# Kernel optimization log

Measured on AMD Instinct MI355X. Metric: run time of the kernel, lower is better.

## Reference

```python
import jax, jax.numpy as jnp
import numpy as np

B_, N, F_ = 8, 2048, 64
H_ = F_ // 2          # hidden state size = 32
DIM = H_ + 2          # LocalGC r/u feature size = 34
NEG = -1e16


def setup_inputs() -> dict:
    key = jax.random.key(0)
    ks = jax.random.split(key, 16)
    xav = lambda k, shp: jax.random.normal(k, shp, jnp.float32) * 0.02
    eye = jnp.eye(N, dtype=jnp.float32)
    A = jnp.maximum((jax.random.uniform(ks[0], (N, N)) < 0.05).astype(jnp.float32), eye)
    Badj = jnp.maximum((jax.random.uniform(ks[1], (N, N)) < 0.05).astype(jnp.float32), eye)
    return dict(
        input=jax.random.normal(ks[2], (B_, N, 2), jnp.float32),
        state=jax.random.normal(ks[3], (B_, N, H_), jnp.float32),
        A=A, Badj=Badj,
        w1c=xav(ks[4], (2, F_, N)), w2c=xav(ks[5], (2, N, N)), biasc=jnp.zeros((2, N, 1)),
        convW=xav(ks[6], (F_, 2)), convb=jnp.zeros((2,)),
        linin_W=xav(ks[7], (2, H_)), linin_b=jnp.zeros((H_,)),
        wr=xav(ks[8], (N, N)), br=jnp.zeros((DIM,)),
        linr_W=xav(ks[9], (DIM, H_)), linr_b=jnp.zeros((H_,)),
        wu=xav(ks[10], (N, N)), bu=jnp.zeros((DIM,)),
        linu_W=xav(ks[11], (DIM, H_)), linu_b=jnp.zeros((H_,)),
        wc=xav(ks[12], (N, N)), bc=jnp.zeros((F_,)),
        linc_W=xav(ks[13], (F_, H_)), linc_b=jnp.zeros((H_,)),
    )


def _local_gc(x, adj, w, b):
    # x: [B,N,D]; out[b,m,d] = sum_n x[b,n,d] * (adj*w)[n,m] + b[d]
    return jnp.einsum('bnd,nm->bmd', x, adj * w) + b


def _core(g, inp, A, Badj, w1c, w2c, biasc, convW, convb):
    # g: [B,N,F] gru_input; inp: [B,N,2] raw cell input (used as 'state' in DoubleDGC)
    demand = jnp.tanh(g @ convW + convb) * 0.5            # [B,N,2]

    def attn(adj, w2, w1, bias):
        h = jnp.einsum('bnf,nm->bmf', g, adj * w2)        # [B,N,F]
        m = jnp.einsum('bmf,fk->bmk', h, w1) + bias       # [B,N,N], bias [N,1] broadcasts
        m = m + NEG * (1.0 - adj)                         # adjacency mask
        return jax.nn.softmax(m, axis=-1)

    mask1 = attn(A, w2c[0], w1c[0], biasc[0])
    mask2 = attn(Badj, w2c[1], w1c[1], biasc[1])
    v = mask1 @ inp[..., :1]                              # [B,N,1]
    q = mask2 @ inp[..., 1:]                              # [B,N,1]
    p = jnp.concatenate([v, q], -1) + demand              # [B,N,2]
    return p


def reference(input, state, A, Badj, w1c, w2c, biasc, convW, convb,
              linin_W, linin_b, wr, br, linr_W, linr_b,
              wu, bu, linu_W, linu_b, wc, bc, linc_W, linc_b):
    x = input @ linin_W + linin_b                         # [B,N,F//2]
    g = jnp.concatenate([x, state], -1)                   # [B,N,F]
    p = _core(g, input, A, Badj, w1c, w2c, biasc, convW, convb)
    fru = jnp.concatenate([p, state], -1)                 # [B,N,DIM]
    r = jax.nn.sigmoid(_local_gc(fru, A, wr, br) @ linr_W + linr_b)
    u = jax.nn.sigmoid(_local_gc(fru, A, wu, bu) @ linu_W + linu_b)
    fc = jnp.concatenate([x, r * state], -1)              # [B,N,F]
    c = jnp.tanh(_local_gc(fc, A, wc, bc) @ linc_W + linc_b)
    H = u * state + (1.0 - u) * c
    return (p, H)
```

## Files before the change

kernel.cpp:

```cpp
#include <hip/hip_runtime.h>
#include <math.h>

#define NN   2048
#define BB   8
#define FF   64
#define HH   32
#define DIMM 34
#define CAP  256

#define G_OFF      0
#define DEM_OFF    (G_OFF + BB*NN*FF)
#define W1T_OFF    (DEM_OFF + BB*NN*2)
#define CNT_OFF    (W1T_OFF + 2*NN*FF)
#define NBRA_OFF   (CNT_OFF + 4*NN)
#define RNBRA_OFF  (NBRA_OFF + NN*CAP)
#define NBRB_OFF   (RNBRA_OFF + NN*CAP)
#define RNBRB_OFF  (NBRB_OFF + NN*CAP)
#define WAW2_OFF   (RNBRB_OFF + NN*CAP)
#define WAR_OFF    (WAW2_OFF + NN*CAP)
#define WAU_OFF    (WAR_OFF + NN*CAP)
#define WAC_OFF    (WAU_OFF + NN*CAP)
#define WBW2_OFF   (WAC_OFF + NN*CAP)
#define U_OFF      (WBW2_OFF + NN*CAP)
#define RS_OFF     (U_OFF + BB*NN*HH)

__global__ void k_pre(const float* __restrict__ in, const float* __restrict__ st,
                      const float* __restrict__ lininW, const float* __restrict__ lininB,
                      const float* __restrict__ convW, const float* __restrict__ convB,
                      float* __restrict__ g, float* __restrict__ dem) {
    int bn = blockIdx.x;
    int f  = threadIdx.x;
    float in0 = in[bn * 2 + 0];
    float in1 = in[bn * 2 + 1];
    float gv;
    if (f < HH) gv = in0 * lininW[f] + in1 * lininW[HH + f] + lininB[f];
    else        gv = st[bn * HH + (f - HH)];
    g[bn * FF + f] = gv;
    float p0 = gv * convW[f * 2 + 0];
    float p1 = gv * convW[f * 2 + 1];
    for (int o = 32; o > 0; o >>= 1) { p0 += __shfl_down(p0, o); p1 += __shfl_down(p1, o); }
    if (f == 0) {
        dem[bn * 2 + 0] = tanhf(p0 + convB[0]) * 0.5f;
        dem[bn * 2 + 1] = tanhf(p1 + convB[1]) * 0.5f;
    }
}

__global__ void k_trans(const float* __restrict__ w1c, float* __restrict__ w1T) {
    int t = blockIdx.x * 256 + threadIdx.x;
    int a   = t >> 17;
    int rem = t & 131071;
    int f   = rem >> 11;
    int k   = rem & 2047;
    w1T[a * (NN * FF) + k * FF + f] = w1c[t];
}

__global__ void k_fill(const float* __restrict__ A, const float* __restrict__ Badj,
                       const float* __restrict__ w2c,
                       const float* __restrict__ wr, const float* __restrict__ wu,
                       const float* __restrict__ wc,
                       int* __restrict__ cnt,
                       int* __restrict__ nbrA, int* __restrict__ rnbrA,
                       int* __restrict__ nbrB, int* __restrict__ rnbrB,
                       float* __restrict__ wAw2, float* __restrict__ wAr,
                       float* __restrict__ wAu, float* __restrict__ wAc,
                       float* __restrict__ wBw2) {
    int gw   = blockIdx.x * 4 + (threadIdx.x >> 6);
    int lane = threadIdx.x & 63;
    int comp = (gw >= NN) ? 1 : 0;
    int n    = comp ? gw - NN : gw;
    const float* row = (comp ? Badj : A) + (size_t)n * NN;

    const float4* r4 = (const float4*)row + lane * 8;
    unsigned int msk = 0;
#pragma unroll
    for (int q = 0; q < 8; ++q) {
        float4 v = r4[q];
        msk |= ((unsigned)(v.x != 0.0f)) << (q * 4 + 0);
        msk |= ((unsigned)(v.y != 0.0f)) << (q * 4 + 1);
        msk |= ((unsigned)(v.z != 0.0f)) << (q * 4 + 2);
        msk |= ((unsigned)(v.w != 0.0f)) << (q * 4 + 3);
    }
    int c    = __popc(msk);
    int incl = c;
#pragma unroll
    for (int o = 1; o < 64; o <<= 1) {
        int tv = __shfl_up(incl, o);
        if (lane >= o) incl += tv;
    }
    int slot  = incl - c;
    int total = __shfl(incl, 63);
    if (lane == 0) cnt[(comp ? 3 * NN : NN) + n] = total;

    int* rnbr   = comp ? rnbrB : rnbrA;
    int* nbr    = comp ? nbrB  : nbrA;
    int  colbase= comp ? 2 * NN : 0;
    unsigned int mm = msk;
    while (mm) {
        int p = __ffs(mm) - 1; mm &= mm - 1;
        int m = lane * 32 + p;
        if (slot < CAP) rnbr[n * CAP + slot] = m;
        slot++;
        int cj = atomicAdd(&cnt[colbase + m], 1);
        if (cj < CAP) {
            size_t tI = (size_t)n * NN + m;
            nbr[m * CAP + cj] = n;
            if (!comp) {
                wAw2[m * CAP + cj] = w2c[tI];
                wAr [m * CAP + cj] = wr[tI];
                wAu [m * CAP + cj] = wu[tI];
                wAc [m * CAP + cj] = wc[tI];
            } else {
                wBw2[m * CAP + cj] = w2c[(size_t)NN * NN + tI];
            }
        }
    }
}

__global__ void __launch_bounds__(512)
k_attn(const float* __restrict__ g, const float* __restrict__ in,
       const float* __restrict__ dem, const float* __restrict__ w1T,
       const float* __restrict__ biasc, const int* __restrict__ cnt,
       const int* __restrict__ nbrA, const float* __restrict__ wAw2,
       const int* __restrict__ rnbrA,
       const int* __restrict__ nbrB, const float* __restrict__ wBw2,
       const int* __restrict__ rnbrB,
       float* __restrict__ pOut) {
    int blk  = blockIdx.x;
    int comp = (blk >= NN) ? 1 : 0;
    int i    = comp ? blk - NN : blk;
    int t    = threadIdx.x;

    const int*   ccnt = cnt + (comp ? 2 * NN : 0);
    const int*   rcnt = cnt + (comp ? 3 * NN : NN);
    const int*   nbr  = comp ? nbrB : nbrA;
    const float* wv   = comp ? wBw2 : wAw2;
    const int*   rnbr = comp ? rnbrB : rnbrA;

    __shared__ float4 hsPart[4][8][16];
    __shared__ float  hs[8][68];

    int cc = ccnt[i]; if (cc > CAP) cc = CAP;
    {
        int f4 = t & 15;
        int b  = (t >> 4) & 7;
        int q  = t >> 7;
        int qlen = (cc + 3) >> 2;
        int jb = q * qlen;
        int je = jb + qlen; if (je > cc) je = cc;
        const float4* gb4 = (const float4*)g + (size_t)b * NN * 16 + f4;
        float4 acc = make_float4(0.f, 0.f, 0.f, 0.f);
        int j = jb;
        for (; j + 4 <= je; j += 4) {
            int   n0 = nbr[i * CAP + j + 0], n1 = nbr[i * CAP + j + 1];
            int   n2 = nbr[i * CAP + j + 2], n3 = nbr[i * CAP + j + 3];
            float w0 = wv[i * CAP + j + 0], w1 = wv[i * CAP + j + 1];
            float w2 = wv[i * CAP + j + 2], w3 = wv[i * CAP + j + 3];
            float4 x0 = gb4[n0 * 16], x1 = gb4[n1 * 16];
            float4 x2 = gb4[n2 * 16], x3 = gb4[n3 * 16];
            acc.x += w0 * x0.x; acc.y += w0 * x0.y; acc.z += w0 * x0.z; acc.w += w0 * x0.w;
            acc.x += w1 * x1.x; acc.y += w1 * x1.y; acc.z += w1 * x1.z; acc.w += w1 * x1.w;
            acc.x += w2 * x2.x; acc.y += w2 * x2.y; acc.z += w2 * x2.z; acc.w += w2 * x2.w;
            acc.x += w3 * x3.x; acc.y += w3 * x3.y; acc.z += w3 * x3.z; acc.w += w3 * x3.w;
        }
        for (; j < je; ++j) {
            int   n = nbr[i * CAP + j];
            float w = wv[i * CAP + j];
            float4 x = gb4[n * 16];
            acc.x += w * x.x; acc.y += w * x.y; acc.z += w * x.z; acc.w += w * x.w;
        }
        hsPart[q][b][f4] = acc;
    }
    __syncthreads();
    if (t < 128) {
        int b2 = t >> 4, f42 = t & 15;
        float4 s0 = hsPart[0][b2][f42], s1 = hsPart[1][b2][f42];
        float4 s2 = hsPart[2][b2][f42], s3 = hsPart[3][b2][f42];
        hs[b2][f42 * 4 + 0] = s0.x + s1.x + s2.x + s3.x;
        hs[b2][f42 * 4 + 1] = s0.y + s1.y + s2.y + s3.y;
        hs[b2][f42 * 4 + 2] = s0.z + s1.z + s2.z + s3.z;
        hs[b2][f42 * 4 + 3] = s0.w + s1.w + s2.w + s3.w;
    }
    __syncthreads();

    int rc = rcnt[i]; if (rc > CAP) rc = CAP;
    int b = t >> 6;
    int s = t & 63;
    float bias = biasc[comp * NN + i];
    int rounds = (rc + 63) >> 6;
    float sc[4]; int nn4[4];
    float lmax = -3.0e38f;
#pragma unroll
    for (int r = 0; r < 4; ++r) {
        float svv = -3.0e38f; int n = 0;
        if (r < rounds) {
            int k = r * 64 + s;
            if (k < rc) {
                n = rnbr[i * CAP + k];
                const float4* w4 = (const float4*)(w1T + ((size_t)comp * NN + n) * FF);
                float acc = bias;
#pragma unroll
                for (int q = 0; q < 16; ++q) {
                    float4 w = w4[q];
                    acc += hs[b][4*q+0] * w.x + hs[b][4*q+1] * w.y
                         + hs[b][4*q+2] * w.z + hs[b][4*q+3] * w.w;
                }
                svv = acc;
            }
        }
        sc[r] = svv; nn4[r] = n;
        lmax = fmaxf(lmax, svv);
    }
#pragma unroll
    for (int o = 32; o > 0; o >>= 1) lmax = fmaxf(lmax, __shfl_xor(lmax, o));
    float num = 0.0f, den = 0.0f;
#pragma unroll
    for (int r = 0; r < 4; ++r) {
        if (r < rounds) {
            int k = r * 64 + s;
            if (k < rc) {
                float e = expf(sc[r] - lmax);
                den += e;
                num += e * in[((size_t)b * NN + nn4[r]) * 2 + comp];
            }
        }
    }
#pragma unroll
    for (int o = 32; o > 0; o >>= 1) { num += __shfl_xor(num, o); den += __shfl_xor(den, o); }
    if (s == 0) {
        size_t bn = (size_t)b * NN + i;
        pOut[bn * 2 + comp] = num / den + dem[bn * 2 + comp];
    }
}

__global__ void __launch_bounds__(512)
k_ru(const float* __restrict__ pOut, const float* __restrict__ st,
     const int* __restrict__ cnt, const int* __restrict__ nbrA,
     const float* __restrict__ wAr, const float* __restrict__ wAu,
     const float* __restrict__ br, const float* __restrict__ bu,
     const float* __restrict__ linrW, const float* __restrict__ linrB,
     const float* __restrict__ linuW, const float* __restrict__ linuB,
     float* __restrict__ ubuf, float* __restrict__ rsbuf) {
    int i = blockIdx.x;
    int t = threadIdx.x;
    int d    = t & 31;
    int b    = (t >> 5) & 7;
    int half = t >> 8;
    __shared__ float LrP[2][8][36], LuP[2][8][36];
    int cc = cnt[i]; if (cc > CAP) cc = CAP;
    int hlen = (cc + 1) >> 1;
    int jb = half * hlen;
    int je = jb + hlen; if (je > cc) je = cc;
    bool dop = (d < 2);
    const float* stb = st + (size_t)b * NN * HH + d;
    const float* pb  = pOut + (size_t)b * NN * 2 + d;
    float ar = 0.f, au = 0.f, arp = 0.f, aup = 0.f;
    int j = jb;
    for (; j + 4 <= je; j += 4) {
        int   n0 = nbrA[i*CAP+j+0], n1 = nbrA[i*CAP+j+1], n2 = nbrA[i*CAP+j+2], n3 = nbrA[i*CAP+j+3];
        float r0 = wAr[i*CAP+j+0], r1 = wAr[i*CAP+j+1], r2 = wAr[i*CAP+j+2], r3 = wAr[i*CAP+j+3];
        float u0 = wAu[i*CAP+j+0], u1 = wAu[i*CAP+j+1], u2 = wAu[i*CAP+j+2], u3 = wAu[i*CAP+j+3];
        float v0 = stb[n0*HH], v1 = stb[n1*HH], v2 = stb[n2*HH], v3 = stb[n3*HH];
        ar += r0*v0 + r1*v1 + r2*v2 + r3*v3;
        au += u0*v0 + u1*v1 + u2*v2 + u3*v3;
        if (dop) {
            float p0 = pb[n0*2], p1 = pb[n1*2], p2 = pb[n2*2], p3 = pb[n3*2];
            arp += r0*p0 + r1*p1 + r2*p2 + r3*p3;
            aup += u0*p0 + u1*p1 + u2*p2 + u3*p3;
        }
    }
    for (; j < je; ++j) {
        int   n  = nbrA[i*CAP+j];
        float r_ = wAr[i*CAP+j];
        float u_ = wAu[i*CAP+j];
        float v  = stb[n*HH];
        ar += r_*v;  au += u_*v;
        if (dop) { float p = pb[n*2]; arp += r_*p; aup += u_*p; }
    }
    LrP[half][b][d + 2] = ar;
    LuP[half][b][d + 2] = au;
    if (dop) { LrP[half][b][d] = arp; LuP[half][b][d] = aup; }
    __syncthreads();
    if (half == 0) {
        float sr = linrB[d], su = linuB[d];
#pragma unroll
        for (int q = 0; q < DIMM; ++q) {
            float lr = LrP[0][b][q] + LrP[1][b][q] + br[q];
            float lu = LuP[0][b][q] + LuP[1][b][q] + bu[q];
            sr += lr * linrW[q * HH + d];
            su += lu * linuW[q * HH + d];
        }
        float r = 1.0f / (1.0f + expf(-sr));
        float u = 1.0f / (1.0f + expf(-su));
        size_t bn = (size_t)b * NN + i;
        rsbuf[bn * HH + d] = r * st[bn * HH + d];
        ubuf [bn * HH + d] = u;
    }
}

__global__ void __launch_bounds__(512)
k_c(const float* __restrict__ g, const float* __restrict__ rsbuf,
    const float* __restrict__ ubuf, const float* __restrict__ st,
    const int* __restrict__ cnt, const int* __restrict__ nbrA,
    const float* __restrict__ wAc, const float* __restrict__ bc,
    const float* __restrict__ lincW, const float* __restrict__ lincB,
    float* __restrict__ Hout) {
    int i = blockIdx.x;
    int t = threadIdx.x;
    int d    = t & 31;
    int b    = (t >> 5) & 7;
    int half = t >> 8;
    __shared__ float LcP[2][8][68];
    int cc = cnt[i]; if (cc > CAP) cc = CAP;
    int hlen = (cc + 1) >> 1;
    int jb = half * hlen;
    int je = jb + hlen; if (je > cc) je = cc;
    const float* gb  = g + (size_t)b * NN * FF + d;
    const float* rsb = rsbuf + (size_t)b * NN * HH + d;
    float a0 = 0.f, a1 = 0.f;
    int j = jb;
    for (; j + 4 <= je; j += 4) {
        int   n0 = nbrA[i*CAP+j+0], n1 = nbrA[i*CAP+j+1], n2 = nbrA[i*CAP+j+2], n3 = nbrA[i*CAP+j+3];
        float w0 = wAc[i*CAP+j+0], w1 = wAc[i*CAP+j+1], w2 = wAc[i*CAP+j+2], w3 = wAc[i*CAP+j+3];
        float x0 = gb[n0*FF],  x1 = gb[n1*FF],  x2 = gb[n2*FF],  x3 = gb[n3*FF];
        float y0 = rsb[n0*HH], y1 = rsb[n1*HH], y2 = rsb[n2*HH], y3 = rsb[n3*HH];
        a0 += w0*x0 + w1*x1 + w2*x2 + w3*x3;
        a1 += w0*y0 + w1*y1 + w2*y2 + w3*y3;
    }
    for (; j < je; ++j) {
        int   n = nbrA[i*CAP+j];
        float w = wAc[i*CAP+j];
        a0 += w * gb[n*FF];
        a1 += w * rsb[n*HH];
    }
    LcP[half][b][d]      = a0;
    LcP[half][b][d + 32] = a1;
    __syncthreads();
    if (half == 0) {
        float sacc = lincB[d];
#pragma unroll
        for (int q = 0; q < FF; ++q) {
            float lc = LcP[0][b][q] + LcP[1][b][q] + bc[q];
            sacc += lc * lincW[q * HH + d];
        }
        float cv = tanhf(sacc);
        size_t bn = (size_t)b * NN + i;
        float u  = ubuf[bn * HH + d];
        float sv = st[bn * HH + d];
        Hout[bn * HH + d] = u * sv + (1.0f - u) * cv;
    }
}

extern "C" void kernel_launch(void* const* d_in, const int* in_sizes, int n_in,
                              void* d_out, int out_size, void* d_ws, size_t ws_size,
                              hipStream_t stream) {
    const float* input  = (const float*)d_in[0];
    const float* state  = (const float*)d_in[1];
    const float* A      = (const float*)d_in[2];
    const float* Badj   = (const float*)d_in[3];
    const float* w1c    = (const float*)d_in[4];
    const float* w2c    = (const float*)d_in[5];
    const float* biasc  = (const float*)d_in[6];
    const float* convW  = (const float*)d_in[7];
    const float* convb  = (const float*)d_in[8];
    const float* lininW = (const float*)d_in[9];
    const float* lininB = (const float*)d_in[10];
    const float* wr     = (const float*)d_in[11];
    const float* br     = (const float*)d_in[12];
    const float* linrW  = (const float*)d_in[13];
    const float* linrB  = (const float*)d_in[14];
    const float* wu     = (const float*)d_in[15];
    const float* bu     = (const float*)d_in[16];
    const float* linuW  = (const float*)d_in[17];
    const float* linuB  = (const float*)d_in[18];
    const float* wc     = (const float*)d_in[19];
    const float* bc     = (const float*)d_in[20];
    const float* lincW  = (const float*)d_in[21];
    const float* lincB  = (const float*)d_in[22];

    float* ws   = (float*)d_ws;
    float* g    = ws + G_OFF;
    float* dem  = ws + DEM_OFF;
    float* w1T  = ws + W1T_OFF;
    int*   cnt  = (int*)(ws + CNT_OFF);
    int*   nbrA = (int*)(ws + NBRA_OFF);
    int*   rnbrA= (int*)(ws + RNBRA_OFF);
    int*   nbrB = (int*)(ws + NBRB_OFF);
    int*   rnbrB= (int*)(ws + RNBRB_OFF);
    float* wAw2 = ws + WAW2_OFF;
    float* wAr  = ws + WAR_OFF;
    float* wAu  = ws + WAU_OFF;
    float* wAc  = ws + WAC_OFF;
    float* wBw2 = ws + WBW2_OFF;
    float* ubuf = ws + U_OFF;
    float* rsbuf= ws + RS_OFF;

    float* pOut = (float*)d_out;
    float* Hout = (float*)d_out + BB * NN * 2;

    hipMemsetAsync(cnt, 0, 4 * NN * sizeof(int), stream);

    k_pre<<<BB * NN, 64, 0, stream>>>(input, state, lininW, lininB, convW, convb, g, dem);
    k_trans<<<(2 * NN * FF) / 256, 256, 0, stream>>>(w1c, w1T);
    k_fill<<<(2 * NN) / 4, 256, 0, stream>>>(A, Badj, w2c, wr, wu, wc, cnt,
                                             nbrA, rnbrA, nbrB, rnbrB,
                                             wAw2, wAr, wAu, wAc, wBw2);
    k_attn<<<2 * NN, 512, 0, stream>>>(g, input, dem, w1T, biasc, cnt,
                                       nbrA, wAw2, rnbrA, nbrB, wBw2, rnbrB, pOut);
    k_ru<<<NN, 512, 0, stream>>>(pOut, state, cnt, nbrA, wAr, wAu, br, bu,
                                 linrW, linrB, linuW, linuB, ubuf, rsbuf);
    k_c<<<NN, 512, 0, stream>>>(g, rsbuf, ubuf, state, cnt, nbrA, wAc, bc,
                                lincW, lincB, Hout);
}
```

Baseline: 483.5 us.

## Double threads per block and stage neighbor lists in shared memory

The attention, r/u and candidate kernels now launch 1024 threads per block instead of 512. Each block first copies its node's neighbor indices and edge weights into shared memory, and the extra threads split the gather over more partitions, which are then reduced. The attention softmax now spans two wave groups, combined through shared max, sum and numerator buffers with extra barriers. The intent is more memory-level parallelism in the latency-bound sparse gathers and fewer redundant global index loads, at the cost of larger blocks, more synchronisation and possibly lower occupancy.

```diff
diff --git a/kernel.cpp b/kernel.cpp
--- a/kernel.cpp
+++ b/kernel.cpp
@@ -116,7 +116,7 @@
     }
 }
 
-__global__ void __launch_bounds__(512)
+__global__ void __launch_bounds__(1024)
 k_attn(const float* __restrict__ g, const float* __restrict__ in,
        const float* __restrict__ dem, const float* __restrict__ w1T,
        const float* __restrict__ biasc, const int* __restrict__ cnt,
@@ -132,29 +132,41 @@
 
     const int*   ccnt = cnt + (comp ? 2 * NN : 0);
     const int*   rcnt = cnt + (comp ? 3 * NN : NN);
-    const int*   nbr  = comp ? nbrB : nbrA;
-    const float* wv   = comp ? wBw2 : wAw2;
-    const int*   rnbr = comp ? rnbrB : rnbrA;
-
-    __shared__ float4 hsPart[4][8][16];
+    const int*   nbrG = comp ? nbrB : nbrA;
+    const float* wvG  = comp ? wBw2 : wAw2;
+    const int*   rnbG = comp ? rnbrB : rnbrA;
+
+    __shared__ int    cnL[CAP];
+    __shared__ float  cwL[CAP];
+    __shared__ int    rnL[CAP];
+    __shared__ float4 hsPart[8][8][16];
     __shared__ float  hs[8][68];
+    __shared__ float  smax[8][2], ssum[8][2], snum[8][2];
 
     int cc = ccnt[i]; if (cc > CAP) cc = CAP;
+    int rc = rcnt[i]; if (rc > CAP) rc = CAP;
+
+    {
+        int k = t & 255, sel = t >> 8;
+        if      (sel == 0) cnL[k] = (k < cc) ? nbrG[i * CAP + k] : 0;
+        else if (sel == 1) cwL[k] = (k < cc) ? wvG [i * CAP + k] : 0.0f;
+        else if (sel == 2) rnL[k] = (k < rc) ? rnbG[i * CAP + k] : 0;
+    }
+    __syncthreads();
+
     {
         int f4 = t & 15;
         int b  = (t >> 4) & 7;
         int q  = t >> 7;
-        int qlen = (cc + 3) >> 2;
+        int qlen = (cc + 7) >> 3;
         int jb = q * qlen;
         int je = jb + qlen; if (je > cc) je = cc;
         const float4* gb4 = (const float4*)g + (size_t)b * NN * 16 + f4;
         float4 acc = make_float4(0.f, 0.f, 0.f, 0.f);
         int j = jb;
         for (; j + 4 <= je; j += 4) {
-            int   n0 = nbr[i * CAP + j + 0], n1 = nbr[i * CAP + j + 1];
-            int   n2 = nbr[i * CAP + j + 2], n3 = nbr[i * CAP + j + 3];
-            float w0 = wv[i * CAP + j + 0], w1 = wv[i * CAP + j + 1];
-            float w2 = wv[i * CAP + j + 2], w3 = wv[i * CAP + j + 3];
+            int   n0 = cnL[j + 0], n1 = cnL[j + 1], n2 = cnL[j + 2], n3 = cnL[j + 3];
+            float w0 = cwL[j + 0], w1 = cwL[j + 1], w2 = cwL[j + 2], w3 = cwL[j + 3];
             float4 x0 = gb4[n0 * 16], x1 = gb4[n1 * 16];
             float4 x2 = gb4[n2 * 16], x3 = gb4[n3 * 16];
             acc.x += w0 * x0.x; acc.y += w0 * x0.y; acc.z += w0 * x0.z; acc.w += w0 * x0.w;
@@ -163,8 +175,8 @@
             acc.x += w3 * x3.x; acc.y += w3 * x3.y; acc.z += w3 * x3.z; acc.w += w3 * x3.w;
         }
         for (; j < je; ++j) {
-            int   n = nbr[i * CAP + j];
-            float w = wv[i * CAP + j];
+            int   n = cnL[j];
+            float w = cwL[j];
             float4 x = gb4[n * 16];
             acc.x += w * x.x; acc.y += w * x.y; acc.z += w * x.z; acc.w += w * x.w;
         }
@@ -173,66 +185,80 @@
     __syncthreads();
     if (t < 128) {
         int b2 = t >> 4, f42 = t & 15;
-        float4 s0 = hsPart[0][b2][f42], s1 = hsPart[1][b2][f42];
-        float4 s2 = hsPart[2][b2][f42], s3 = hsPart[3][b2][f42];
-        hs[b2][f42 * 4 + 0] = s0.x + s1.x + s2.x + s3.x;
-        hs[b2][f42 * 4 + 1] = s0.y + s1.y + s2.y + s3.y;
-        hs[b2][f42 * 4 + 2] = s0.z + s1.z + s2.z + s3.z;
-        hs[b2][f42 * 4 + 3] = s0.w + s1.w + s2.w + s3.w;
-    }
-    __syncthreads();
-
-    int rc = rcnt[i]; if (rc > CAP) rc = CAP;
-    int b = t >> 6;
-    int s = t & 63;
+        float4 s = hsPart[0][b2][f42];
+#pragma unroll
+        for (int q = 1; q < 8; ++q) {
+            float4 p = hsPart[q][b2][f42];
+            s.x += p.x; s.y += p.y; s.z += p.z; s.w += p.w;
+        }
+        hs[b2][f42 * 4 + 0] = s.x;
+        hs[b2][f42 * 4 + 1] = s.y;
+        hs[b2][f42 * 4 + 2] = s.z;
+        hs[b2][f42 * 4 + 3] = s.w;
+    }
+    __syncthreads();
+
+    int s  = t & 63;
+    int wI = t >> 6;
+    int b  = wI & 7;
+    int rr = wI >> 3;
     float bias = biasc[comp * NN + i];
-    int rounds = (rc + 63) >> 6;
-    float sc[4]; int nn4[4];
-    float lmax = -3.0e38f;
-#pragma unroll
-    for (int r = 0; r < 4; ++r) {
-        float svv = -3.0e38f; int n = 0;
-        if (r < rounds) {
-            int k = r * 64 + s;
-            if (k < rc) {
-                n = rnbr[i * CAP + k];
-                const float4* w4 = (const float4*)(w1T + ((size_t)comp * NN + n) * FF);
-                float acc = bias;
-#pragma unroll
-                for (int q = 0; q < 16; ++q) {
-                    float4 w = w4[q];
-                    acc += hs[b][4*q+0] * w.x + hs[b][4*q+1] * w.y
-                         + hs[b][4*q+2] * w.z + hs[b][4*q+3] * w.w;
-                }
-                svv = acc;
-            }
-        }
-        sc[r] = svv; nn4[r] = n;
-        lmax = fmaxf(lmax, svv);
-    }
+    int k0 = rr * 64 + s;
+    int k1 = (rr + 2) * 64 + s;
+    float sc0 = -3.0e38f, sc1 = -3.0e38f;
+    int n0 = 0, n1 = 0;
+    if (k0 < rc) {
+        n0 = rnL[k0];
+        const float4* w4 = (const float4*)(w1T + ((size_t)comp * NN + n0) * FF);
+        float a = bias;
+#pragma unroll
+        for (int q = 0; q < 16; ++q) {
+            float4 w = w4[q];
+            a += hs[b][4*q+0]*w.x + hs[b][4*q+1]*w.y + hs[b][4*q+2]*w.z + hs[b][4*q+3]*w.w;
+        }
+        sc0 = a;
+    }
+    if (k1 < rc) {
+        n1 = rnL[k1];
+        const float4* w4 = (const float4*)(w1T + ((size_t)comp * NN + n1) * FF);
+        float a = bias;
+#pragma unroll
+        for (int q = 0; q < 16; ++q) {
+            float4 w = w4[q];
+            a += hs[b][4*q+0]*w.x + hs[b][4*q+1]*w.y + hs[b][4*q+2]*w.z + hs[b][4*q+3]*w.w;
+        }
+        sc1 = a;
+    }
+    float lmax = fmaxf(sc0, sc1);
 #pragma unroll
     for (int o = 32; o > 0; o >>= 1) lmax = fmaxf(lmax, __shfl_xor(lmax, o));
+    if (s == 0) smax[b][rr] = lmax;
+    __syncthreads();
+    float gmax = fmaxf(smax[b][0], smax[b][1]);
     float num = 0.0f, den = 0.0f;
-#pragma unroll
-    for (int r = 0; r < 4; ++r) {
-        if (r < rounds) {
-            int k = r * 64 + s;
-            if (k < rc) {
-                float e = expf(sc[r] - lmax);
-                den += e;
-                num += e * in[((size_t)b * NN + nn4[r]) * 2 + comp];
-            }
-        }
+    if (k0 < rc) {
+        float e = expf(sc0 - gmax);
+        den += e;
+        num += e * in[((size_t)b * NN + n0) * 2 + comp];
+    }
+    if (k1 < rc) {
+        float e = expf(sc1 - gmax);
+        den += e;
+        num += e * in[((size_t)b * NN + n1) * 2 + comp];
     }
 #pragma unroll
     for (int o = 32; o > 0; o >>= 1) { num += __shfl_xor(num, o); den += __shfl_xor(den, o); }
-    if (s == 0) {
+    if (s == 0) { ssum[b][rr] = den; snum[b][rr] = num; }
+    __syncthreads();
+    if (rr == 0 && s == 0) {
+        float td = ssum[b][0] + ssum[b][1];
+        float tn = snum[b][0] + snum[b][1];
         size_t bn = (size_t)b * NN + i;
-        pOut[bn * 2 + comp] = num / den + dem[bn * 2 + comp];
-    }
-}
-
-__global__ void __launch_bounds__(512)
+        pOut[bn * 2 + comp] = tn / td + dem[bn * 2 + comp];
+    }
+}
+
+__global__ void __launch_bounds__(1024)
 k_ru(const float* __restrict__ pOut, const float* __restrict__ st,
      const int* __restrict__ cnt, const int* __restrict__ nbrA,
      const float* __restrict__ wAr, const float* __restrict__ wAu,
@@ -242,23 +268,32 @@
      float* __restrict__ ubuf, float* __restrict__ rsbuf) {
     int i = blockIdx.x;
     int t = threadIdx.x;
-    int d    = t & 31;
-    int b    = (t >> 5) & 7;
-    int half = t >> 8;
-    __shared__ float LrP[2][8][36], LuP[2][8][36];
+    int d = t & 31;
+    int b = (t >> 5) & 7;
+    int q = t >> 8;
+    __shared__ int   cnL[CAP];
+    __shared__ float cwrL[CAP], cwuL[CAP];
+    __shared__ float LrP[4][8][36], LuP[4][8][36];
     int cc = cnt[i]; if (cc > CAP) cc = CAP;
-    int hlen = (cc + 1) >> 1;
-    int jb = half * hlen;
-    int je = jb + hlen; if (je > cc) je = cc;
+    {
+        int k = t & 255, sel = t >> 8;
+        if      (sel == 0) cnL [k] = (k < cc) ? nbrA[i * CAP + k] : 0;
+        else if (sel == 1) cwrL[k] = (k < cc) ? wAr [i * CAP + k] : 0.0f;
+        else if (sel == 2) cwuL[k] = (k < cc) ? wAu [i * CAP + k] : 0.0f;
+    }
+    __syncthreads();
+    int qlen = (cc + 3) >> 2;
+    int jb = q * qlen;
+    int je = jb + qlen; if (je > cc) je = cc;
     bool dop = (d < 2);
     const float* stb = st + (size_t)b * NN * HH + d;
     const float* pb  = pOut + (size_t)b * NN * 2 + d;
     float ar = 0.f, au = 0.f, arp = 0.f, aup = 0.f;
     int j = jb;
     for (; j + 4 <= je; j += 4) {
-        int   n0 = nbrA[i*CAP+j+0], n1 = nbrA[i*CAP+j+1], n2 = nbrA[i*CAP+j+2], n3 = nbrA[i*CAP+j+3];
-        float r0 = wAr[i*CAP+j+0], r1 = wAr[i*CAP+j+1], r2 = wAr[i*CAP+j+2], r3 = wAr[i*CAP+j+3];
-        float u0 = wAu[i*CAP+j+0], u1 = wAu[i*CAP+j+1], u2 = wAu[i*CAP+j+2], u3 = wAu[i*CAP+j+3];
+        int   n0 = cnL[j+0], n1 = cnL[j+1], n2 = cnL[j+2], n3 = cnL[j+3];
+        float r0 = cwrL[j+0], r1 = cwrL[j+1], r2 = cwrL[j+2], r3 = cwrL[j+3];
+        float u0 = cwuL[j+0], u1 = cwuL[j+1], u2 = cwuL[j+2], u3 = cwuL[j+3];
         float v0 = stb[n0*HH], v1 = stb[n1*HH], v2 = stb[n2*HH], v3 = stb[n3*HH];
         ar += r0*v0 + r1*v1 + r2*v2 + r3*v3;
         au += u0*v0 + u1*v1 + u2*v2 + u3*v3;
@@ -269,25 +304,25 @@
         }
     }
     for (; j < je; ++j) {
-        int   n  = nbrA[i*CAP+j];
-        float r_ = wAr[i*CAP+j];
-        float u_ = wAu[i*CAP+j];
+        int   n  = cnL[j];
+        float r_ = cwrL[j];
+        float u_ = cwuL[j];
         float v  = stb[n*HH];
         ar += r_*v;  au += u_*v;
         if (dop) { float p = pb[n*2]; arp += r_*p; aup += u_*p; }
     }
-    LrP[half][b][d + 2] = ar;
-    LuP[half][b][d + 2] = au;
-    if (dop) { LrP[half][b][d] = arp; LuP[half][b][d] = aup; }
-    __syncthreads();
-    if (half == 0) {
+    LrP[q][b][d + 2] = ar;
+    LuP[q][b][d + 2] = au;
+    if (dop) { LrP[q][b][d] = arp; LuP[q][b][d] = aup; }
+    __syncthreads();
+    if (q == 0) {
         float sr = linrB[d], su = linuB[d];
 #pragma unroll
-        for (int q = 0; q < DIMM; ++q) {
-            float lr = LrP[0][b][q] + LrP[1][b][q] + br[q];
-            float lu = LuP[0][b][q] + LuP[1][b][q] + bu[q];
-            sr += lr * linrW[q * HH + d];
-            su += lu * linuW[q * HH + d];
+        for (int k = 0; k < DIMM; ++k) {
+            float lr = LrP[0][b][k] + LrP[1][b][k] + LrP[2][b][k] + LrP[3][b][k] + br[k];
+            float lu = LuP[0][b][k] + LuP[1][b][k] + LuP[2][b][k] + LuP[3][b][k] + bu[k];
+            sr += lr * linrW[k * HH + d];
+            su += lu * linuW[k * HH + d];
         }
         float r = 1.0f / (1.0f + expf(-sr));
         float u = 1.0f / (1.0f + expf(-su));
@@ -297,7 +332,7 @@
     }
 }
 
-__global__ void __launch_bounds__(512)
+__global__ void __launch_bounds__(1024)
 k_c(const float* __restrict__ g, const float* __restrict__ rsbuf,
     const float* __restrict__ ubuf, const float* __restrict__ st,
     const int* __restrict__ cnt, const int* __restrict__ nbrA,
@@ -306,41 +341,49 @@
     float* __restrict__ Hout) {
     int i = blockIdx.x;
     int t = threadIdx.x;
-    int d    = t & 31;
-    int b    = (t >> 5) & 7;
-    int half = t >> 8;
-    __shared__ float LcP[2][8][68];
+    int d = t & 31;
+    int b = (t >> 5) & 7;
+    int q = t >> 8;
+    __shared__ int   cnL[CAP];
+    __shared__ float cwcL[CAP];
+    __shared__ float LcP[4][8][68];
     int cc = cnt[i]; if (cc > CAP) cc = CAP;
-    int hlen = (cc + 1) >> 1;
-    int jb = half * hlen;
-    int je = jb + hlen; if (je > cc) je = cc;
+    {
+        int k = t & 255, sel = t >> 8;
+        if      (sel == 0) cnL [k] = (k < cc) ? nbrA[i * CAP + k] : 0;
+        else if (sel == 1) cwcL[k] = (k < cc) ? wAc [i * CAP + k] : 0.0f;
+    }
+    __syncthreads();
+    int qlen = (cc + 3) >> 2;
+    int jb = q * qlen;
+    int je = jb + qlen; if (je > cc) je = cc;
     const float* gb  = g + (size_t)b * NN * FF + d;
     const float* rsb = rsbuf + (size_t)b * NN * HH + d;
     float a0 = 0.f, a1 = 0.f;
     int j = jb;
     for (; j + 4 <= je; j += 4) {
-        int   n0 = nbrA[i*CAP+j+0], n1 = nbrA[i*CAP+j+1], n2 = nbrA[i*CAP+j+2], n3 = nbrA[i*CAP+j+3];
-        float w0 = wAc[i*CAP+j+0], w1 = wAc[i*CAP+j+1], w2 = wAc[i*CAP+j+2], w3 = wAc[i*CAP+j+3];
+        int   n0 = cnL[j+0], n1 = cnL[j+1], n2 = cnL[j+2], n3 = cnL[j+3];
+        float w0 = cwcL[j+0], w1 = cwcL[j+1], w2 = cwcL[j+2], w3 = cwcL[j+3];
         float x0 = gb[n0*FF],  x1 = gb[n1*FF],  x2 = gb[n2*FF],  x3 = gb[n3*FF];
         float y0 = rsb[n0*HH], y1 = rsb[n1*HH], y2 = rsb[n2*HH], y3 = rsb[n3*HH];
         a0 += w0*x0 + w1*x1 + w2*x2 + w3*x3;
         a1 += w0*y0 + w1*y1 + w2*y2 + w3*y3;
     }
     for (; j < je; ++j) {
-        int   n = nbrA[i*CAP+j];
-        float w = wAc[i*CAP+j];
+        int   n = cnL[j];
+        float w = cwcL[j];
         a0 += w * gb[n*FF];
         a1 += w * rsb[n*HH];
     }
-    LcP[half][b][d]      = a0;
-    LcP[half][b][d + 32] = a1;
-    __syncthreads();
-    if (half == 0) {
+    LcP[q][b][d]      = a0;
+    LcP[q][b][d + 32] = a1;
+    __syncthreads();
+    if (q == 0) {
         float sacc = lincB[d];
 #pragma unroll
-        for (int q = 0; q < FF; ++q) {
-            float lc = LcP[0][b][q] + LcP[1][b][q] + bc[q];
-            sacc += lc * lincW[q * HH + d];
+        for (int k = 0; k < FF; ++k) {
+            float lc = LcP[0][b][k] + LcP[1][b][k] + LcP[2][b][k] + LcP[3][b][k] + bc[k];
+            sacc += lc * lincW[k * HH + d];
         }
         float cv = tanhf(sacc);
         size_t bn = (size_t)b * NN + i;
@@ -404,10 +447,10 @@
     k_fill<<<(2 * NN) / 4, 256, 0, stream>>>(A, Badj, w2c, wr, wu, wc, cnt,
                                              nbrA, rnbrA, nbrB, rnbrB,
                                              wAw2, wAr, wAu, wAc, wBw2);
-    k_attn<<<2 * NN, 512, 0, stream>>>(g, input, dem, w1T, biasc, cnt,
-                                       nbrA, wAw2, rnbrA, nbrB, wBw2, rnbrB, pOut);
-    k_ru<<<NN, 512, 0, stream>>>(pOut, state, cnt, nbrA, wAr, wAu, br, bu,
-                                 linrW, linrB, linuW, linuB, ubuf, rsbuf);
-    k_c<<<NN, 512, 0, stream>>>(g, rsbuf, ubuf, state, cnt, nbrA, wAc, bc,
-                                lincW, lincB, Hout);
-}
+    k_attn<<<2 * NN, 1024, 0, stream>>>(g, input, dem, w1T, biasc, cnt,
+                                        nbrA, wAw2, rnbrA, nbrB, wBw2, rnbrB, pOut);
+    k_ru<<<NN, 1024, 0, stream>>>(pOut, state, cnt, nbrA, wAr, wAu, br, bu,
+                                  linrW, linrB, linuW, linuB, ubuf, rsbuf);
+    k_c<<<NN, 1024, 0, stream>>>(g, rsbuf, ubuf, state, cnt, nbrA, wAc, bc,
+                                 lincW, lincB, Hout);
+}
```

New measurement: 473.7 us. 2.0% less time.
